# Performance work log

Measured on AMD Instinct MI355X. Metric: run time of the kernel, lower is better.

## Reference

```python
import jax, jax.numpy as jnp
import numpy as np

L, H, P = 16384, 1024, 512  # seq len, model width, state size (conj_sym: P = ssm_size//2)
DT_MIN, DT_MAX = 1e-3, 1e-1
STEP_RESCALE = 1.0


def setup_inputs() -> dict:
    key = jax.random.key(0)
    ks = jax.random.split(key, 7)
    input_sequence = jax.random.normal(ks[0], (L, H), dtype=jnp.float32)
    # Lambda: stable diagonal (Re < 0), like DPLR-HiPPO (Re = -0.5, spread imag parts)
    Lambda_re = -0.5 - jax.random.uniform(ks[1], (P,), dtype=jnp.float32)
    Lambda_im = 10.0 * jax.random.normal(ks[2], (P,), dtype=jnp.float32)
    # B (P,H,2) and C (H,P,2): real/imag stacked parameterization
    B = jax.random.normal(ks[3], (P, H, 2), dtype=jnp.float32) / np.float32(np.sqrt(H))
    C = jax.random.normal(ks[4], (H, P, 2), dtype=jnp.float32) / np.float32(np.sqrt(P))
    D = jax.random.normal(ks[5], (H,), dtype=jnp.float32)
    log_step = (jax.random.uniform(ks[6], (P, 1), dtype=jnp.float32)
                * (np.log(DT_MAX) - np.log(DT_MIN)) + np.log(DT_MIN)).astype(jnp.float32)
    return {"input_sequence": input_sequence, "Lambda_re": Lambda_re,
            "Lambda_im": Lambda_im, "B": B, "C": C, "D": D, "log_step": log_step}


def _binop(q_i, q_j):
    # diagonal linear recurrence composition; elementwise, so works on stacked arrays
    A_i, b_i = q_i
    A_j, b_j = q_j
    return (A_j * A_i, A_j * b_i + b_j)


def reference(input_sequence, Lambda_re, Lambda_im, B, C, D, log_step):
    Lambda = Lambda_re + 1j * Lambda_im                      # (P,) complex64
    B_tilde = B[..., 0] + 1j * B[..., 1]                     # (P,H)
    C_tilde = C[..., 0] + 1j * C[..., 1]                     # (H,P)
    Delta = STEP_RESCALE * jnp.exp(log_step[:, 0])           # (P,)
    # ZOH discretization
    Lambda_bar = jnp.exp(Lambda * Delta)                     # (P,)
    B_bar = ((Lambda_bar - 1.0) / Lambda)[:, None] * B_tilde # (P,H)
    # per-step scan elements
    Lambda_elements = jnp.broadcast_to(Lambda_bar, (input_sequence.shape[0], P))
    Bu_elements = jnp.einsum('lh,ph->lp', input_sequence, B_bar)  # (L,P) complex
    _, xs = jax.lax.associative_scan(_binop, (Lambda_elements, Bu_elements))
    # conj_sym readout: 2 * Re(C x)
    ys = 2.0 * jnp.einsum('lp,hp->lh', xs, C_tilde).real     # (L,H) float32
    return ys + input_sequence * D
```

## Files before the change

kernel.cpp:

```cpp
#include <hip/hip_runtime.h>
#include <math.h>

#define LL 16384
#define HH 1024
#define PP 512
#define NP2 1024
#define CHUNK 64
#define NCHUNK 256

#define BM2 256
#define BN2 256
#define SUBK 32
#define REG_U16 16384

typedef unsigned short u16;
typedef __attribute__((ext_vector_type(8))) short bf16x8;
typedef __attribute__((ext_vector_type(4))) float f32x4;

__device__ __forceinline__ u16 f2bf(float f) {
    unsigned u = __float_as_uint(f);
    unsigned r = 0x7fffu + ((u >> 16) & 1u);
    return (u16)((u + r) >> 16);
}
__device__ __forceinline__ float bf2f(u16 x) {
    return __uint_as_float(((unsigned)x) << 16);
}

__device__ __forceinline__ void gload_lds16(const void* g, void* l) {
    __builtin_amdgcn_global_load_lds(
        (const __attribute__((address_space(1))) unsigned int*)g,
        (__attribute__((address_space(3))) unsigned int*)l, 16, 0, 0);
}

#define SB0 __builtin_amdgcn_sched_barrier(0)

__global__ __launch_bounds__(256) void k_prep(
        const float* __restrict__ B, const float* __restrict__ C,
        const float* __restrict__ u, const float* __restrict__ lre,
        const float* __restrict__ lim, const float* __restrict__ logstep,
        u16* __restrict__ bb, u16* __restrict__ cp, u16* __restrict__ ub,
        float* __restrict__ lbre, float* __restrict__ lbim,
        float* __restrict__ ltre, float* __restrict__ ltim) {
    const int bx = blockIdx.x;
    if (bx < 2048) {
        int t = bx * 256 + threadIdx.x;
        int p = t >> 10, h = t & 1023;
        float2 b = ((const float2*)B)[t];
        float dt = expf(logstep[p]);
        float ar = lre[p], ai = lim[p];
        float e = expf(ar * dt);
        float s, c;
        sincosf(ai * dt, &s, &c);
        float nr = e * c - 1.0f, ni = e * s;
        float den = ar * ar + ai * ai;
        float gr = (nr * ar + ni * ai) / den;
        float gi = (ni * ar - nr * ai) / den;
        bb[(size_t)(2 * p) * HH + h]     = f2bf(gr * b.x - gi * b.y);
        bb[(size_t)(2 * p + 1) * HH + h] = f2bf(gr * b.y + gi * b.x);
    } else if (bx < 4096) {
        int t = (bx - 2048) * 256 + threadIdx.x;
        int h = t >> 9, p = t & 511;
        float2 c = ((const float2*)C)[t];
        cp[(size_t)h * NP2 + 2 * p]     = f2bf(c.x);
        cp[(size_t)h * NP2 + 2 * p + 1] = f2bf(-c.y);
    } else if (bx < 20480) {
        size_t i = ((size_t)(bx - 4096) * 256 + threadIdx.x) * 4;
        float4 v = *(const float4*)&u[i];
        unsigned lo = (unsigned)f2bf(v.x) | ((unsigned)f2bf(v.y) << 16);
        unsigned hi = (unsigned)f2bf(v.z) | ((unsigned)f2bf(v.w) << 16);
        *(uint2*)&ub[i] = make_uint2(lo, hi);
    } else {
        int p = (bx - 20480) * 256 + threadIdx.x;
        if (p < PP) {
            float dt = expf(logstep[p]);
            float ar = lre[p], ai = lim[p];
            float e = expf(ar * dt);
            float s, c;
            sincosf(ai * dt, &s, &c);
            float Lr = e * c, Li = e * s;
            lbre[p] = Lr; lbim[p] = Li;
            float tr = Lr, ti = Li;
            for (int i6 = 0; i6 < 6; i6++) {
                float rr = tr * tr - ti * ti;
                float mm = 2.0f * tr * ti;
                tr = rr; ti = mm;
            }
            ltre[p] = tr; ltim[p] = ti;
        }
    }
}

template<int FUSE>
__global__ __launch_bounds__(512, 2) void k_gemm2(
        const u16* __restrict__ A, const u16* __restrict__ Bt,
        void* __restrict__ outp, const int K,
        const u16* __restrict__ ubf, const float* __restrict__ Din,
        const float* __restrict__ lbre, const float* __restrict__ lbim,
        float* __restrict__ frO, float* __restrict__ fiO) {
    extern __shared__ u16 smem[];
    const int b = blockIdx.x;
    const int xcd = b & 7, sidx = b >> 3;
    const int m0 = (xcd * 8 + (sidx >> 2)) * BM2;
    const int n0 = (sidx & 3) * BN2;
    const int t = threadIdx.x;
    const int lane = t & 63, wid = t >> 6;
    const int wm = (wid >> 2) * 128, wn = (wid & 3) * 64;
    const int frow = lane & 15, quad = (lane >> 4) & 3;

    f32x4 acc[8][4];
    #pragma unroll
    for (int i = 0; i < 8; i++)
        #pragma unroll
        for (int j = 0; j < 4; j++) acc[i][j] = (f32x4){0.f, 0.f, 0.f, 0.f};

    const int sr = t >> 2, slot = t & 3;
    const int seg = slot ^ ((sr >> 1) & 3);
    const u16* gA = A + (size_t)(m0 + sr) * K + seg * 8;
    const u16* gB = Bt + (size_t)(n0 + sr) * K + seg * 8;
    const int ldst = sr * 32 + slot * 8;

    const int aoff = (wm + frow) * 32 + ((quad ^ ((frow >> 1) & 3)) * 8);
    const int boff = (wn + frow) * 32 + ((quad ^ ((frow >> 1) & 3)) * 8);

    const int NT = K / SUBK;

    {
        u16* d0 = smem + ldst;
        gload_lds16(gA,                     d0);
        gload_lds16(gA + (size_t)128 * K,   d0 + 4096);
        gload_lds16(gB,                     d0 + 8192);
        gload_lds16(gB + (size_t)128 * K,   d0 + 12288);
        u16* d1 = smem + REG_U16 + ldst;
        gload_lds16(gA + SUBK,                   d1);
        gload_lds16(gA + (size_t)128 * K + SUBK, d1 + 4096);
        gload_lds16(gB + SUBK,                   d1 + 8192);
        gload_lds16(gB + (size_t)128 * K + SUBK, d1 + 12288);
    }
    asm volatile("s_waitcnt vmcnt(4)" ::: "memory");
    SB0;
    __builtin_amdgcn_s_barrier();
    SB0;

    int rc = 0;
    int rs = 2;
    for (int s = 0; s < NT; ++s) {
        const u16* Ar = smem + rc * REG_U16;
        const u16* Br = Ar + 8192;
        const bool do_stage = (s + 2 < NT);
        const u16* gAs = gA + (size_t)(s + 2) * SUBK;
        const u16* gBs = gB + (size_t)(s + 2) * SUBK;
        u16* dS = smem + rs * REG_U16 + ldst;

        bf16x8 av0 = *(const bf16x8*)&Ar[aoff + 0 * 512];
        bf16x8 av1 = *(const bf16x8*)&Ar[aoff + 1 * 512];
        bf16x8 av2 = *(const bf16x8*)&Ar[aoff + 2 * 512];
        bf16x8 av3 = *(const bf16x8*)&Ar[aoff + 3 * 512];
        bf16x8 bv0 = *(const bf16x8*)&Br[boff + 0 * 512];
        bf16x8 bv1 = *(const bf16x8*)&Br[boff + 1 * 512];
        bf16x8 bv2 = *(const bf16x8*)&Br[boff + 2 * 512];
        bf16x8 bv3 = *(const bf16x8*)&Br[boff + 3 * 512];
        if (do_stage) {
            gload_lds16(gAs,                   dS);
            gload_lds16(gAs + (size_t)128 * K, dS + 4096);
        }
        SB0;
        __builtin_amdgcn_s_barrier();
        asm volatile("s_waitcnt lgkmcnt(0)" ::: "memory");
        SB0;
        __builtin_amdgcn_s_setprio(1);
        acc[0][0] = __builtin_amdgcn_mfma_f32_16x16x32_bf16(av0, bv0, acc[0][0], 0, 0, 0);
        acc[0][1] = __builtin_amdgcn_mfma_f32_16x16x32_bf16(av0, bv1, acc[0][1], 0, 0, 0);
        acc[0][2] = __builtin_amdgcn_mfma_f32_16x16x32_bf16(av0, bv2, acc[0][2], 0, 0, 0);
        acc[0][3] = __builtin_amdgcn_mfma_f32_16x16x32_bf16(av0, bv3, acc[0][3], 0, 0, 0);
        acc[1][0] = __builtin_amdgcn_mfma_f32_16x16x32_bf16(av1, bv0, acc[1][0], 0, 0, 0);
        acc[1][1] = __builtin_amdgcn_mfma_f32_16x16x32_bf16(av1, bv1, acc[1][1], 0, 0, 0);
        acc[1][2] = __builtin_amdgcn_mfma_f32_16x16x32_bf16(av1, bv2, acc[1][2], 0, 0, 0);
        acc[1][3] = __builtin_amdgcn_mfma_f32_16x16x32_bf16(av1, bv3, acc[1][3], 0, 0, 0);
        acc[2][0] = __builtin_amdgcn_mfma_f32_16x16x32_bf16(av2, bv0, acc[2][0], 0, 0, 0);
        acc[2][1] = __builtin_amdgcn_mfma_f32_16x16x32_bf16(av2, bv1, acc[2][1], 0, 0, 0);
        acc[2][2] = __builtin_amdgcn_mfma_f32_16x16x32_bf16(av2, bv2, acc[2][2], 0, 0, 0);
        acc[2][3] = __builtin_amdgcn_mfma_f32_16x16x32_bf16(av2, bv3, acc[2][3], 0, 0, 0);
        acc[3][0] = __builtin_amdgcn_mfma_f32_16x16x32_bf16(av3, bv0, acc[3][0], 0, 0, 0);
        acc[3][1] = __builtin_amdgcn_mfma_f32_16x16x32_bf16(av3, bv1, acc[3][1], 0, 0, 0);
        acc[3][2] = __builtin_amdgcn_mfma_f32_16x16x32_bf16(av3, bv2, acc[3][2], 0, 0, 0);
        acc[3][3] = __builtin_amdgcn_mfma_f32_16x16x32_bf16(av3, bv3, acc[3][3], 0, 0, 0);
        __builtin_amdgcn_s_setprio(0);
        SB0;
        __builtin_amdgcn_s_barrier();
        SB0;

        bf16x8 av4 = *(const bf16x8*)&Ar[aoff + 4 * 512];
        bf16x8 av5 = *(const bf16x8*)&Ar[aoff + 5 * 512];
        bf16x8 av6 = *(const bf16x8*)&Ar[aoff + 6 * 512];
        bf16x8 av7 = *(const bf16x8*)&Ar[aoff + 7 * 512];
        if (do_stage) {
            gload_lds16(gBs,                   dS + 8192);
            gload_lds16(gBs + (size_t)128 * K, dS + 12288);
        }
        SB0;
        __builtin_amdgcn_s_barrier();
        asm volatile("s_waitcnt lgkmcnt(0)" ::: "memory");
        SB0;
        __builtin_amdgcn_s_setprio(1);
        acc[4][0] = __builtin_amdgcn_mfma_f32_16x16x32_bf16(av4, bv0, acc[4][0], 0, 0, 0);
        acc[4][1] = __builtin_amdgcn_mfma_f32_16x16x32_bf16(av4, bv1, acc[4][1], 0, 0, 0);
        acc[4][2] = __builtin_amdgcn_mfma_f32_16x16x32_bf16(av4, bv2, acc[4][2], 0, 0, 0);
        acc[4][3] = __builtin_amdgcn_mfma_f32_16x16x32_bf16(av4, bv3, acc[4][3], 0, 0, 0);
        acc[5][0] = __builtin_amdgcn_mfma_f32_16x16x32_bf16(av5, bv0, acc[5][0], 0, 0, 0);
        acc[5][1] = __builtin_amdgcn_mfma_f32_16x16x32_bf16(av5, bv1, acc[5][1], 0, 0, 0);
        acc[5][2] = __builtin_amdgcn_mfma_f32_16x16x32_bf16(av5, bv2, acc[5][2], 0, 0, 0);
        acc[5][3] = __builtin_amdgcn_mfma_f32_16x16x32_bf16(av5, bv3, acc[5][3], 0, 0, 0);
        acc[6][0] = __builtin_amdgcn_mfma_f32_16x16x32_bf16(av6, bv0, acc[6][0], 0, 0, 0);
        acc[6][1] = __builtin_amdgcn_mfma_f32_16x16x32_bf16(av6, bv1, acc[6][1], 0, 0, 0);
        acc[6][2] = __builtin_amdgcn_mfma_f32_16x16x32_bf16(av6, bv2, acc[6][2], 0, 0, 0);
        acc[6][3] = __builtin_amdgcn_mfma_f32_16x16x32_bf16(av6, bv3, acc[6][3], 0, 0, 0);
        acc[7][0] = __builtin_amdgcn_mfma_f32_16x16x32_bf16(av7, bv0, acc[7][0], 0, 0, 0);
        acc[7][1] = __builtin_amdgcn_mfma_f32_16x16x32_bf16(av7, bv1, acc[7][1], 0, 0, 0);
        acc[7][2] = __builtin_amdgcn_mfma_f32_16x16x32_bf16(av7, bv2, acc[7][2], 0, 0, 0);
        acc[7][3] = __builtin_amdgcn_mfma_f32_16x16x32_bf16(av7, bv3, acc[7][3], 0, 0, 0);
        __builtin_amdgcn_s_setprio(0);
        if (s < NT - 2)       asm volatile("s_waitcnt vmcnt(4)" ::: "memory");
        else if (s == NT - 2) asm volatile("s_waitcnt vmcnt(0)" ::: "memory");
        SB0;
        __builtin_amdgcn_s_barrier();
        SB0;

        rc = (rc == 2) ? 0 : rc + 1;
        rs = (rs == 2) ? 0 : rs + 1;
    }

    if (FUSE) {
        float* smf = (float*)smem;
        float* Cout = (float*)outp;
        #pragma unroll
        for (int h = 0; h < 2; h++) {
            if ((wid >> 2) == h) {
                #pragma unroll
                for (int i = 0; i < 8; i++)
                    #pragma unroll
                    for (int j = 0; j < 4; j++) {
                        f32x4 v = acc[i][j];
                        #pragma unroll
                        for (int r = 0; r < 4; r++)
                            smf[(i * 16 + quad * 4 + r) * 256 + wn + j * 16 + frow]
                                = v[r];
                    }
            }
            __syncthreads();
            #pragma unroll
            for (int k = 0; k < 16; k++) {
                const int l = t + k * 512;
                const int row = l >> 6, c4 = (l & 63) * 4;
                const size_t o = (size_t)(m0 + h * 128 + row) * 1024 + n0 + c4;
                float4 s4 = ((const float4*)smf)[l];
                uint2 uv = *(const uint2*)&ubf[o];
                float4 dv = *(const float4*)&Din[n0 + c4];
                float4 r4;
                r4.x = 2.0f * s4.x + bf2f((u16)(uv.x & 0xffff)) * dv.x;
                r4.y = 2.0f * s4.y + bf2f((u16)(uv.x >> 16))    * dv.y;
                r4.z = 2.0f * s4.z + bf2f((u16)(uv.y & 0xffff)) * dv.z;
                r4.w = 2.0f * s4.w + bf2f((u16)(uv.y >> 16))    * dv.w;
                *(float4*)&Cout[o] = r4;
            }
            __syncthreads();
        }
    } else {
        u16* Cb = (u16*)outp;
        unsigned* sm32 = (unsigned*)smem;
        #pragma unroll
        for (int i = 0; i < 8; i++)
            #pragma unroll
            for (int j = 0; j < 4; j++) {
                f32x4 v = acc[i][j];
                #pragma unroll
                for (int r = 0; r < 4; r++)
                    smem[(wm + i * 16 + quad * 4 + r) * 256 + wn + j * 16 + frow]
                        = f2bf(v[r]);
            }
        __syncthreads();
        #pragma unroll
        for (int k = 0; k < 16; k++) {
            const int l = t + k * 512;
            const int row = l >> 5, c16 = (l & 31) * 8;
            *(uint4*)&Cb[(size_t)(m0 + row) * 1024 + n0 + c16] =
                ((const uint4*)smem)[l];
        }
        const int ch = t >> 7, q = t & 127;
        const int sp = (n0 >> 1) + q;
        const float sar = lbre[sp], sai = lbim[sp];
        float xr = 0.f, xi = 0.f;
        #pragma unroll 8
        for (int r = 0; r < 64; r++) {
            unsigned v = sm32[(ch * 64 + r) * 128 + q];
            float br = bf2f((u16)(v & 0xffff));
            float bi = bf2f((u16)(v >> 16));
            float nr = sar * xr - sai * xi + br;
            float ni = sar * xi + sai * xr + bi;
            xr = nr; xi = ni;
        }
        frO[((m0 >> 6) + ch) * PP + sp] = xr;
        fiO[((m0 >> 6) + ch) * PP + sp] = xi;
    }
}

__global__ __launch_bounds__(256) void k_scan2(
        const float* __restrict__ fr, const float* __restrict__ fi,
        const float* __restrict__ ltre, const float* __restrict__ ltim,
        float* __restrict__ cr, float* __restrict__ ci) {
    __shared__ float Ar[NCHUNK], Ai[NCHUNK], br[NCHUNK], bi[NCHUNK];
    const int p = blockIdx.x;
    const int c = threadIdx.x;
    const float lr = ltre[p], li = ltim[p];
    Ar[c] = lr; Ai[c] = li;
    br[c] = fr[c * PP + p];
    bi[c] = fi[c * PP + p];
    __syncthreads();
    #pragma unroll
    for (int d = 1; d < NCHUNK; d <<= 1) {
        float pAr = 0.f, pAi = 0.f, pbr = 0.f, pbi = 0.f;
        const bool has = (c >= d);
        if (has) { pAr = Ar[c-d]; pAi = Ai[c-d]; pbr = br[c-d]; pbi = bi[c-d]; }
        float cAr = Ar[c], cAi = Ai[c], cbr = br[c], cbi = bi[c];
        __syncthreads();
        if (has) {
            Ar[c] = cAr * pAr - cAi * pAi;
            Ai[c] = cAr * pAi + cAi * pAr;
            br[c] = cAr * pbr - cAi * pbi + cbr;
            bi[c] = cAr * pbi + cAi * pbr + cbi;
        }
        __syncthreads();
    }
    cr[c * PP + p] = (c == 0) ? 0.f : br[c-1];
    ci[c * PP + p] = (c == 0) ? 0.f : bi[c-1];
}

__global__ void k_scan3(unsigned* __restrict__ bu,
                        const float* __restrict__ lbre, const float* __restrict__ lbim,
                        const float* __restrict__ cr, const float* __restrict__ ci) {
    int p = blockIdx.x * 256 + threadIdx.x;
    int c = blockIdx.y;
    float ar = lbre[p], ai = lbim[p];
    float xr = cr[c * PP + p], xi = ci[c * PP + p];
    unsigned* b = bu + (size_t)c * CHUNK * PP + p;
    for (int j = 0; j < CHUNK; j += 8) {
        unsigned vv[8];
        #pragma unroll
        for (int q = 0; q < 8; q++) vv[q] = b[q * PP];
        unsigned w[8];
        #pragma unroll
        for (int q = 0; q < 8; q++) {
            float br = bf2f((u16)(vv[q] & 0xffff));
            float bi = bf2f((u16)(vv[q] >> 16));
            float nr = ar * xr - ai * xi + br;
            float ni = ar * xi + ai * xr + bi;
            xr = nr; xi = ni;
            w[q] = (unsigned)f2bf(xr) | ((unsigned)f2bf(xi) << 16);
        }
        #pragma unroll
        for (int q = 0; q < 8; q++) b[q * PP] = w[q];
        b += 8 * PP;
    }
}

extern "C" void kernel_launch(void* const* d_in, const int* in_sizes, int n_in,
                              void* d_out, int out_size, void* d_ws, size_t ws_size,
                              hipStream_t stream) {
    const float* u       = (const float*)d_in[0];
    const float* lre     = (const float*)d_in[1];
    const float* lim     = (const float*)d_in[2];
    const float* B       = (const float*)d_in[3];
    const float* C       = (const float*)d_in[4];
    const float* D       = (const float*)d_in[5];
    const float* logstep = (const float*)d_in[6];
    float* out = (float*)d_out;

    float* w = (float*)d_ws;
    float* lbre = w + 1024;
    float* lbim = w + 1536;
    float* ltre = w + 2048;
    float* ltim = w + 2560;
    float* fr   = w + 4096;
    float* fi   = fr + NCHUNK * PP;
    float* cr   = fi + NCHUNK * PP;
    float* ci   = cr + NCHUNK * PP;
    u16*   bub  = (u16*)(w + (1 << 20));
    u16*   ub   = bub + (size_t)LL * NP2;
    u16*   bb   = ub + (size_t)LL * HH;
    u16*   cp   = bb + (size_t)NP2 * HH;

    static int attr_done = 0;
    if (!attr_done) {
        hipFuncSetAttribute(reinterpret_cast<const void*>(k_gemm2<0>),
                            hipFuncAttributeMaxDynamicSharedMemorySize, 131072);
        hipFuncSetAttribute(reinterpret_cast<const void*>(k_gemm2<1>),
                            hipFuncAttributeMaxDynamicSharedMemorySize, 131072);
        attr_done = 1;
    }

    k_prep<<<20482, 256, 0, stream>>>(B, C, u, lre, lim, logstep,
                                      bb, cp, ub, lbre, lbim, ltre, ltim);
    k_gemm2<0><<<(NP2 / BN2) * (LL / BM2), 512, 131072, stream>>>(
        ub, bb, bub, HH, nullptr, nullptr, lbre, lbim, fr, fi);
    k_scan2<<<PP, NCHUNK, 0, stream>>>(fr, fi, ltre, ltim, cr, ci);
    k_scan3<<<dim3(PP / 256, NCHUNK), 256, 0, stream>>>(
        (unsigned*)bub, lbre, lbim, cr, ci);
    k_gemm2<1><<<(HH / BN2) * (LL / BM2), 512, 131072, stream>>>(
        bub, cp, out, NP2, ub, D, nullptr, nullptr, nullptr, nullptr);
}
```

Before: 233.3 us.

## Fold chunk-carry prefix scan into scan3 via redundant sequential recomputation

Removes the separate k_scan2 kernel, which did a log-step parallel prefix over chunk summaries per state. Each k_scan3 thread now serially recomputes the carry-in for its chunk by iterating over all preceding chunk summaries with the chunk-level decay. This saves one kernel launch and the cr/ci round trip through memory. In exchange it adds redundant work that grows linearly with chunk index, up to 255 dependent complex FMAs plus loads per thread for late chunks.

```diff
diff --git a/kernel.cpp b/kernel.cpp
--- a/kernel.cpp
+++ b/kernel.cpp
@@ -303,44 +303,36 @@
     }
 }
 
-__global__ __launch_bounds__(256) void k_scan2(
-        const float* __restrict__ fr, const float* __restrict__ fi,
-        const float* __restrict__ ltre, const float* __restrict__ ltim,
-        float* __restrict__ cr, float* __restrict__ ci) {
-    __shared__ float Ar[NCHUNK], Ai[NCHUNK], br[NCHUNK], bi[NCHUNK];
-    const int p = blockIdx.x;
-    const int c = threadIdx.x;
-    const float lr = ltre[p], li = ltim[p];
-    Ar[c] = lr; Ai[c] = li;
-    br[c] = fr[c * PP + p];
-    bi[c] = fi[c * PP + p];
-    __syncthreads();
-    #pragma unroll
-    for (int d = 1; d < NCHUNK; d <<= 1) {
-        float pAr = 0.f, pAi = 0.f, pbr = 0.f, pbi = 0.f;
-        const bool has = (c >= d);
-        if (has) { pAr = Ar[c-d]; pAi = Ai[c-d]; pbr = br[c-d]; pbi = bi[c-d]; }
-        float cAr = Ar[c], cAi = Ai[c], cbr = br[c], cbi = bi[c];
-        __syncthreads();
-        if (has) {
-            Ar[c] = cAr * pAr - cAi * pAi;
-            Ai[c] = cAr * pAi + cAi * pAr;
-            br[c] = cAr * pbr - cAi * pbi + cbr;
-            bi[c] = cAr * pbi + cAi * pbr + cbi;
-        }
-        __syncthreads();
-    }
-    cr[c * PP + p] = (c == 0) ? 0.f : br[c-1];
-    ci[c * PP + p] = (c == 0) ? 0.f : bi[c-1];
-}
-
 __global__ void k_scan3(unsigned* __restrict__ bu,
                         const float* __restrict__ lbre, const float* __restrict__ lbim,
-                        const float* __restrict__ cr, const float* __restrict__ ci) {
+                        const float* __restrict__ fr, const float* __restrict__ fi,
+                        const float* __restrict__ ltre, const float* __restrict__ ltim) {
     int p = blockIdx.x * 256 + threadIdx.x;
     int c = blockIdx.y;
+    const float lr = ltre[p], li = ltim[p];
+    float xr = 0.f, xi = 0.f;
+    int c0 = 0;
+    for (; c0 + 8 <= c; c0 += 8) {
+        float br8[8], bi8[8];
+        #pragma unroll
+        for (int q = 0; q < 8; q++) {
+            br8[q] = fr[(c0 + q) * PP + p];
+            bi8[q] = fi[(c0 + q) * PP + p];
+        }
+        #pragma unroll
+        for (int q = 0; q < 8; q++) {
+            float nr = lr * xr - li * xi + br8[q];
+            float ni = lr * xi + li * xr + bi8[q];
+            xr = nr; xi = ni;
+        }
+    }
+    for (; c0 < c; c0++) {
+        float b1r = fr[c0 * PP + p], b1i = fi[c0 * PP + p];
+        float nr = lr * xr - li * xi + b1r;
+        float ni = lr * xi + li * xr + b1i;
+        xr = nr; xi = ni;
+    }
     float ar = lbre[p], ai = lbim[p];
-    float xr = cr[c * PP + p], xi = ci[c * PP + p];
     unsigned* b = bu + (size_t)c * CHUNK * PP + p;
     for (int j = 0; j < CHUNK; j += 8) {
         unsigned vv[8];
@@ -381,8 +373,6 @@
     float* ltim = w + 2560;
     float* fr   = w + 4096;
     float* fi   = fr + NCHUNK * PP;
-    float* cr   = fi + NCHUNK * PP;
-    float* ci   = cr + NCHUNK * PP;
     u16*   bub  = (u16*)(w + (1 << 20));
     u16*   ub   = bub + (size_t)LL * NP2;
     u16*   bb   = ub + (size_t)LL * HH;
@@ -401,9 +391,8 @@
                                       bb, cp, ub, lbre, lbim, ltre, ltim);
     k_gemm2<0><<<(NP2 / BN2) * (LL / BM2), 512, 131072, stream>>>(
         ub, bb, bub, HH, nullptr, nullptr, lbre, lbim, fr, fi);
-    k_scan2<<<PP, NCHUNK, 0, stream>>>(fr, fi, ltre, ltim, cr, ci);
     k_scan3<<<dim3(PP / 256, NCHUNK), 256, 0, stream>>>(
-        (unsigned*)bub, lbre, lbim, cr, ci);
+        (unsigned*)bub, lbre, lbim, fr, fi, ltre, ltim);
     k_gemm2<1><<<(HH / BN2) * (LL / BM2), 512, 131072, stream>>>(
         bub, cp, out, NP2, ub, D, nullptr, nullptr, nullptr, nullptr);
 }
```

Result: no change. 235.2 us (+0.8%).
